# Kernel tuning notes

Hardware: AMD Instinct MI355X
Metric: run time of the kernel (lower is better)

## Reference

```python
import jax, jax.numpy as jnp
import numpy as np
from jax import lax


def setup_inputs() -> dict:
    key = jax.random.key(0)
    ks = jax.random.split(key, 5)
    B, N, F = 16, 2048, 64
    S, P, O = 4, 22, 42  # n_dimensions, n_propagate, n_filters
    x = jax.random.normal(ks[0], (B, N, F), dtype=jnp.float32)
    W_s = jax.random.normal(ks[1], (F, S), dtype=jnp.float32) * (1.0 / np.sqrt(F))
    b_s = jnp.zeros((S,), dtype=jnp.float32)
    W_f = jax.random.normal(ks[2], (F, P), dtype=jnp.float32) * (1.0 / np.sqrt(F))
    b_f = jnp.zeros((P,), dtype=jnp.float32)
    W_o = jax.random.normal(ks[3], (F + 2 * P, O), dtype=jnp.float32) * (1.0 / np.sqrt(F + 2 * P))
    b_o = jnp.zeros((O,), dtype=jnp.float32)
    return {"x": x, "W_s": W_s, "b_s": b_s, "W_f": W_f, "b_f": b_f,
            "W_o": W_o, "b_o": b_o, "n_neighbours": 40}


def reference(x, W_s, b_s, W_f, b_f, W_o, b_o, n_neighbours):
    # x: [B, N, F]
    coords = x @ W_s + b_s            # [B, N, S]   spatial transform
    feats = x @ W_f + b_f             # [B, N, P]   feature transform (FLR)
    # pairwise squared distances: [B, N, N]
    d2 = jnp.sum((coords[:, :, None, :] - coords[:, None, :, :]) ** 2, axis=-1)
    # k nearest (top_k of -distance); drop self (slot 0)
    neg_d, idx = lax.top_k(-d2, n_neighbours)        # [B, N, k]
    dist = -neg_d[:, :, 1:]                          # [B, N, k-1]
    nbr_idx = idx[:, :, 1:]                          # [B, N, k-1]
    weights = jnp.exp(-dist)[..., None]              # [B, N, k-1, 1]
    # batched gather of neighbour features: [B, N, k-1, P]
    nbr_feats = jax.vmap(lambda f, i: f[i])(feats, nbr_idx)
    weighted = nbr_feats * weights
    n_max = jnp.max(weighted, axis=2)                # [B, N, P]
    n_mean = jnp.mean(weighted, axis=2)              # [B, N, P]
    updated = jnp.concatenate([x, n_max, n_mean], axis=-1)  # [B, N, F+2P]
    return jnp.tanh(updated @ W_o + b_o)             # [B, N, n_filters]
```

## Files before the change

kernel.cpp:

```cpp
#include <hip/hip_runtime.h>
#include <math.h>

#define BB 16
#define NN 2048
#define FF 64
#define SS 4
#define PP 22
#define OO 42
#define FPDIM (FF + 2*PP)
#define NREG 32
#define PREBLK 128
#define XWOBLK ((BB*NN*21 + 255)/256)

__device__ __forceinline__ float readfirstlane_f32(float v) {
    return __uint_as_float((unsigned)__builtin_amdgcn_readfirstlane((int)__float_as_uint(v)));
}

__device__ __forceinline__ int wave_scan_dpp(int x) {
    x += __builtin_amdgcn_update_dpp(0, x, 0x111, 0xf, 0xf, true);
    x += __builtin_amdgcn_update_dpp(0, x, 0x112, 0xf, 0xf, true);
    x += __builtin_amdgcn_update_dpp(0, x, 0x114, 0xf, 0xf, true);
    x += __builtin_amdgcn_update_dpp(0, x, 0x118, 0xf, 0xf, true);
    x += __builtin_amdgcn_update_dpp(0, x, 0x142, 0xa, 0xf, true);
    x += __builtin_amdgcn_update_dpp(0, x, 0x143, 0xc, 0xf, true);
    return x;
}
__device__ __forceinline__ int wave_sum_dpp(int x) {
    return __builtin_amdgcn_readlane(wave_scan_dpp(x), 63);
}
__device__ __forceinline__ float wave_fsum_dpp(float x) {
    float t;
    t = __uint_as_float((unsigned)__builtin_amdgcn_update_dpp(0, (int)__float_as_uint(x), 0x111, 0xf, 0xf, true)); x += t;
    t = __uint_as_float((unsigned)__builtin_amdgcn_update_dpp(0, (int)__float_as_uint(x), 0x112, 0xf, 0xf, true)); x += t;
    t = __uint_as_float((unsigned)__builtin_amdgcn_update_dpp(0, (int)__float_as_uint(x), 0x114, 0xf, 0xf, true)); x += t;
    t = __uint_as_float((unsigned)__builtin_amdgcn_update_dpp(0, (int)__float_as_uint(x), 0x118, 0xf, 0xf, true)); x += t;
    t = __uint_as_float((unsigned)__builtin_amdgcn_update_dpp(0, (int)__float_as_uint(x), 0x142, 0xa, 0xf, true)); x += t;
    t = __uint_as_float((unsigned)__builtin_amdgcn_update_dpp(0, (int)__float_as_uint(x), 0x143, 0xc, 0xf, true)); x += t;
    return __uint_as_float((unsigned)__builtin_amdgcn_readlane((int)__float_as_uint(x), 63));
}

__global__ __launch_bounds__(256) void prep_kernel(
    const float* __restrict__ x, const float* __restrict__ Ws, const float* __restrict__ bs,
    const float* __restrict__ Wf, const float* __restrict__ bf,
    const float* __restrict__ Wo, const float* __restrict__ bo,
    float* __restrict__ coords, float* __restrict__ feats, float* __restrict__ xwo)
{
    if (blockIdx.x >= PREBLK) {
        int idx = (blockIdx.x - PREBLK) * 256 + threadIdx.x;
        if (idx >= BB * NN * 21) return;
        int row = idx / 21;
        int p   = idx - row * 21;
        int o   = p * 2;
        const float4* xr = (const float4*)(x + (size_t)row * FF);
        float a0 = bo[o], b0 = bo[o + 1], a1 = 0.f, b1 = 0.f;
        #pragma unroll
        for (int k4 = 0; k4 < FF / 4; k4++) {
            float4 xv = xr[k4];
            const float* wb = Wo + (k4 * 4) * OO + o;
            float2 w0 = *((const float2*)(wb));
            float2 w1 = *((const float2*)(wb + OO));
            float2 w2 = *((const float2*)(wb + 2 * OO));
            float2 w3 = *((const float2*)(wb + 3 * OO));
            a0 = fmaf(xv.x, w0.x, a0); b0 = fmaf(xv.x, w0.y, b0);
            a1 = fmaf(xv.y, w1.x, a1); b1 = fmaf(xv.y, w1.y, b1);
            a0 = fmaf(xv.z, w2.x, a0); b0 = fmaf(xv.z, w2.y, b0);
            a1 = fmaf(xv.w, w3.x, a1); b1 = fmaf(xv.w, w3.y, b1);
        }
        *((float2*)(xwo + (size_t)idx * 2)) = make_float2(a0 + a1, b0 + b1);
        return;
    }

    int row = blockIdx.x * 256 + threadIdx.x;
    if (row >= BB * NN) return;

    const float4* x4 = (const float4*)(x + (size_t)row * FF);
    float c0 = bs[0], c1 = bs[1], c2 = bs[2], c3 = bs[3];
    float f[PP];
    #pragma unroll
    for (int c = 0; c < PP; c++) f[c] = bf[c];

    #pragma unroll
    for (int k4 = 0; k4 < FF / 4; k4++) {
        float4 xv = x4[k4];
        float xs[4] = {xv.x, xv.y, xv.z, xv.w};
        #pragma unroll
        for (int r = 0; r < 4; r++) {
            int k = k4 * 4 + r;
            float xk = xs[r];
            c0 = fmaf(xk, Ws[k * SS + 0], c0);
            c1 = fmaf(xk, Ws[k * SS + 1], c1);
            c2 = fmaf(xk, Ws[k * SS + 2], c2);
            c3 = fmaf(xk, Ws[k * SS + 3], c3);
            #pragma unroll
            for (int c = 0; c < PP; c++) f[c] = fmaf(xk, Wf[k * PP + c], f[c]);
        }
    }
    float4* cp = (float4*)(coords + (size_t)row * SS);
    *cp = make_float4(c0, c1, c2, c3);
    float* fo = feats + (size_t)row * PP;
    #pragma unroll
    for (int c = 0; c < PP; c++) fo[c] = f[c];
}

__global__ __launch_bounds__(128, 4) void knn_out_kernel(
    const float* __restrict__ coords, const float* __restrict__ feats,
    const float* __restrict__ xwo, const float* __restrict__ Wo,
    const int* __restrict__ nnbr, float* __restrict__ out)
{
    const int lane = threadIdx.x & 63;
    const int w    = threadIdx.x >> 6;
    const int q    = blockIdx.x * 2 + w;
    const int b    = q >> 11;
    const int i    = q & (NN - 1);

    int K = *nnbr; K = K < 2 ? 2 : (K > 64 ? 64 : K);

    __shared__ int   isel[2][64];
    __shared__ float wsel[2][64];
    __shared__ unsigned long long candk[2][64];
    __shared__ __align__(16) float urow[2][48];

    float xw = 0.f;
    if (lane < OO) xw = xwo[(size_t)q * OO + lane];

    const float4* cb = (const float4*)(coords + (size_t)b * NN * SS);
    float4 qv = cb[i];
    const float qx = readfirstlane_f32(qv.x);
    const float qy = readfirstlane_f32(qv.y);
    const float qz = readfirstlane_f32(qv.z);
    const float qw = readfirstlane_f32(qv.w);

    float d2r[NREG];
    float lmin = INFINITY;
    #pragma unroll 4
    for (int r = 0; r < NREG; r++) {
        float4 c = cb[r * 64 + lane];
        float d0 = qx - c.x, d1 = qy - c.y, d2 = qz - c.z, d3 = qw - c.w;
        float v = d0 * d0 + d1 * d1 + d2 * d2 + d3 * d3;
        d2r[r] = v;
        lmin = fminf(lmin, v);
    }

    float t0 = wave_fsum_dpp(lmin) * (1.0f / 64.0f);

    unsigned loU = 0u, hiU = 0x7F800000u;
    int cLo = 0, cHi = NN;
    int laneLo = 0, laneHi = NREG;
    float tPrev = t0; int cPrev = -1;

    if (t0 > 1e-30f) {
        float t1 = t0 * 0.75f, t2 = t0 * 0.95f, t3 = t0 * 1.15f, t4 = t0 * 1.40f;
        int l1 = 0, l2 = 0, l3 = 0, l4 = 0;
        #pragma unroll
        for (int r = 0; r < NREG; r++) {
            float v = d2r[r];
            l1 += (v < t1) ? 1 : 0;
            l2 += (v < t2) ? 1 : 0;
            l3 += (v < t3) ? 1 : 0;
            l4 += (v < t4) ? 1 : 0;
        }
        int s12 = wave_sum_dpp(l1 | (l2 << 16));
        int s34 = wave_sum_dpp(l3 | (l4 << 16));
        int c1 = s12 & 0xFFFF, c2 = s12 >> 16, c3 = s34 & 0xFFFF, c4 = s34 >> 16;
        if (c1 >= K)      { hiU = __float_as_uint(t1); cHi = c1; laneHi = l1; }
        else if (c2 >= K) { loU = __float_as_uint(t1); cLo = c1; laneLo = l1;
                            hiU = __float_as_uint(t2); cHi = c2; laneHi = l2; }
        else if (c3 >= K) { loU = __float_as_uint(t2); cLo = c2; laneLo = l2;
                            hiU = __float_as_uint(t3); cHi = c3; laneHi = l3; }
        else if (c4 >= K) { loU = __float_as_uint(t3); cLo = c3; laneLo = l3;
                            hiU = __float_as_uint(t4); cHi = c4; laneHi = l4; }
        else              { loU = __float_as_uint(t4); cLo = c4; laneLo = l4; }
        int bc = -1, bd = 0x7FFFFFFF; float bt = t0;
        int cs[4] = {c1, c2, c3, c4}; float ts[4] = {t1, t2, t3, t4};
        #pragma unroll
        for (int u = 0; u < 4; u++) {
            int d = cs[u] > K ? cs[u] - K : K - cs[u];
            if (cs[u] > 0 && d < bd) { bd = d; bc = cs[u]; bt = ts[u]; }
        }
        if (bc > 0) { tPrev = bt; cPrev = bc; }
        else        { tPrev = t4; cPrev = 0; }
    }

    int probes = 0;
    while (cHi - cLo > 64 && hiU - loU > 1u && probes < 20) {
        unsigned tAU = 0u, tBU = 0u;
        bool fell = false;
        if (cPrev > 0) {
            float g = tPrev * __fsqrt_rn((float)K / (float)cPrev);
            tAU = __float_as_uint(g * 0.88f); tBU = __float_as_uint(g * 1.18f);
        } else if (cPrev == 0) {
            tAU = __float_as_uint(tPrev * 3.0f); tBU = __float_as_uint(tPrev * 9.0f);
        } else fell = true;
        unsigned span = hiU - loU;
        if (fell || !(tAU > loU && tAU < hiU)) tAU = loU + span / 3u;
        if (tAU <= loU) tAU = loU + 1u;
        if (tAU >= hiU) tAU = hiU - 1u;
        if (fell || !(tBU >= tAU && tBU < hiU)) tBU = tAU + (hiU - tAU) / 2u;
        if (tBU < tAU) tBU = tAU;
        if (tBU >= hiU) tBU = hiU - 1u;

        float tA = __uint_as_float(tAU), tB = __uint_as_float(tBU);
        int clA = 0, clB = 0;
        #pragma unroll
        for (int r = 0; r < NREG; r++) {
            clA += (d2r[r] < tA) ? 1 : 0;
            clB += (d2r[r] < tB) ? 1 : 0;
        }
        int tot = wave_sum_dpp(clA | (clB << 16));
        int cA = tot & 0xFFFF, cB = tot >> 16;

        if (cA >= K) { hiU = tAU; cHi = cA; laneHi = clA; }
        else {
            loU = tAU; cLo = cA; laneLo = clA;
            if (cB >= K) { hiU = tBU; cHi = cB; laneHi = clB; }
            else         { loU = tBU; cLo = cB; laneLo = clB; }
        }
        int dA = cA > K ? cA - K : K - cA;
        int dB = cB > K ? cB - K : K - cB;
        if (cA > 0 && dA <= dB) { tPrev = tA; cPrev = cA; }
        else                    { tPrev = tB; cPrev = cB; }
        probes++;
    }

    const float lo = __uint_as_float(loU);
    const float hi = __uint_as_float(hiU);
    const int  need = K - cLo;

    int c1c = laneLo;
    int c2c = laneHi - laneLo;
    if (lane == (i & 63) && loU > 0u) c1c -= 1;
    int pk = c1c | (c2c << 16);
    int inc = wave_scan_dpp(pk);
    int excl = inc - pk;
    int tot  = __builtin_amdgcn_readlane(inc, 63);
    int b1 = excl & 0xFFFF;
    int b2 = excl >> 16;
    const int nbelow = tot & 0xFFFF;
    int ecand = tot >> 16; if (ecand > 64) ecand = 64;
    #pragma unroll
    for (int r = 0; r < NREG; r++) {
        float v = d2r[r];
        int j = r * 64 + lane;
        if ((v < lo) & (j != i)) { isel[w][b1] = j; wsel[w][b1] = v; b1++; }
        else if ((v >= lo) & (v < hi)) { if (b2 < 64) candk[w][b2] = ((unsigned long long)__float_as_uint(v) << 32) | (unsigned)j; b2++; }
    }
    __builtin_amdgcn_wave_barrier();

    int nsel;
    if (ecand == need && loU > 0u) {
        if (lane < ecand) {
            int slot = nbelow + lane;
            if (slot < 64) {
                unsigned long long k2 = candk[w][lane];
                isel[w][slot] = (int)(k2 & 0xFFFFFFFFull);
                wsel[w][slot] = __uint_as_float((unsigned)(k2 >> 32));
            }
        }
        nsel = nbelow + ecand;
        if (nsel > 64) nsel = 64;
    } else {
        unsigned long long mykey = ~0ull;
        if (lane < ecand) mykey = candk[w][lane];
        int mr = 0;
        for (int u = 0; u < ecand; u++) {
            unsigned long long k2 = candk[w][u];
            mr += (k2 < mykey) ? 1 : 0;
        }
        int mj = (int)(mykey & 0xFFFFFFFFull);
        bool ps = (lane < ecand) & (mr < need) & (mj != i);
        unsigned long long ms = __ballot(ps);
        if (ps) {
            int slot = nbelow + __popcll(ms & ((1ull << lane) - 1ull));
            if (slot < 64) { isel[w][slot] = mj; wsel[w][slot] = __uint_as_float((unsigned)(mykey >> 32)); }
        }
        nsel = nbelow + __popcll(ms);
        if (nsel > 64) nsel = 64;
    }
    __builtin_amdgcn_wave_barrier();
    if (lane < nsel) wsel[w][lane] = __expf(-wsel[w][lane]);
    __builtin_amdgcn_wave_barrier();

    const float* fb = feats + (size_t)b * NN * PP;
    int g = lane >> 5, c = lane & 31;
    float mx = -INFINITY, sm = 0.f;
    if (c < PP) {
        #pragma unroll 8
        for (int m = g; m < nsel; m += 2) {
            int j = isel[w][m]; float wt = wsel[w][m];
            float f = fb[(size_t)j * PP + c];
            float wf = wt * f;
            mx = fmaxf(mx, wf); sm += wf;
        }
    }
    float mx2 = __shfl_xor(mx, 32, 64);
    float sm2 = __shfl_xor(sm, 32, 64);
    mx = fmaxf(mx, mx2); sm += sm2;
    if (g == 0 && c < PP) {
        urow[w][c]      = mx;
        urow[w][PP + c] = sm / (float)(K - 1);
    }
    __builtin_amdgcn_wave_barrier();

    if (lane < OO) {
        float a0 = xw, a1 = 0.f, a2 = 0.f, a3 = 0.f;
        const float* wo = Wo + FF * OO + lane;
        #pragma unroll
        for (int k4 = 0; k4 < (2 * PP) / 4; k4++) {
            float4 u = *((const float4*)&urow[w][k4 * 4]);
            a0 = fmaf(u.x, wo[(k4 * 4 + 0) * OO], a0);
            a1 = fmaf(u.y, wo[(k4 * 4 + 1) * OO], a1);
            a2 = fmaf(u.z, wo[(k4 * 4 + 2) * OO], a2);
            a3 = fmaf(u.w, wo[(k4 * 4 + 3) * OO], a3);
        }
        float acc = (a0 + a1) + (a2 + a3);
        float a = acc < -12.f ? -12.f : (acc > 12.f ? 12.f : acc);
        float e2 = __expf(2.f * a);
        out[(size_t)q * OO + lane] = (e2 - 1.f) / (e2 + 1.f);
    }
}

extern "C" void kernel_launch(void* const* d_in, const int* in_sizes, int n_in,
                              void* d_out, int out_size, void* d_ws, size_t ws_size,
                              hipStream_t stream) {
    const float* x  = (const float*)d_in[0];
    const float* Ws = (const float*)d_in[1];
    const float* bs = (const float*)d_in[2];
    const float* Wf = (const float*)d_in[3];
    const float* bf = (const float*)d_in[4];
    const float* Wo = (const float*)d_in[5];
    const float* bo = (const float*)d_in[6];
    const int*   nn = (const int*)d_in[7];
    float* out = (float*)d_out;

    float* coords = (float*)d_ws;
    float* feats  = coords + (size_t)BB * NN * SS;
    float* xwo    = feats  + (size_t)BB * NN * PP;

    prep_kernel<<<PREBLK + XWOBLK, 256, 0, stream>>>(x, Ws, bs, Wf, bf, Wo, bo, coords, feats, xwo);
    knn_out_kernel<<<(BB * NN) / 2, 128, 0, stream>>>(coords, feats, xwo, Wo, nn, out);
}
```

Baseline: 183.2 us.

## Replace threshold probing with ballot-compacted candidate list and in-register bisection

Reworks the per-query k-nearest selection. A single pass over the register distances compacts every candidate under a coarse threshold into a shared list of up to 256 packed (distance, index) keys using ballot and mbcnt. The threshold is refined by interpolation and bisection over only those few candidates held in registers, instead of repeated full 2048-element count passes with DPP reductions. Selected neighbours are stored as packed keys with precomputed feature offsets, which merges the index and weight arrays. The risk is extra capture iterations over all distances when the initial threshold guess yields fewer than K or more than 256 candidates.

```diff
diff --git a/kernel.cpp b/kernel.cpp
--- a/kernel.cpp
+++ b/kernel.cpp
@@ -9,6 +9,7 @@
 #define OO 42
 #define FPDIM (FF + 2*PP)
 #define NREG 32
+#define CAP 256
 #define PREBLK 128
 #define XWOBLK ((BB*NN*21 + 255)/256)
 
@@ -16,18 +17,11 @@
     return __uint_as_float((unsigned)__builtin_amdgcn_readfirstlane((int)__float_as_uint(v)));
 }
 
-__device__ __forceinline__ int wave_scan_dpp(int x) {
-    x += __builtin_amdgcn_update_dpp(0, x, 0x111, 0xf, 0xf, true);
-    x += __builtin_amdgcn_update_dpp(0, x, 0x112, 0xf, 0xf, true);
-    x += __builtin_amdgcn_update_dpp(0, x, 0x114, 0xf, 0xf, true);
-    x += __builtin_amdgcn_update_dpp(0, x, 0x118, 0xf, 0xf, true);
-    x += __builtin_amdgcn_update_dpp(0, x, 0x142, 0xa, 0xf, true);
-    x += __builtin_amdgcn_update_dpp(0, x, 0x143, 0xc, 0xf, true);
-    return x;
-}
-__device__ __forceinline__ int wave_sum_dpp(int x) {
-    return __builtin_amdgcn_readlane(wave_scan_dpp(x), 63);
-}
+__device__ __forceinline__ int lane_prefix(unsigned long long m) {
+    return __builtin_amdgcn_mbcnt_hi((unsigned)(m >> 32),
+           __builtin_amdgcn_mbcnt_lo((unsigned)m, 0u));
+}
+
 __device__ __forceinline__ float wave_fsum_dpp(float x) {
     float t;
     t = __uint_as_float((unsigned)__builtin_amdgcn_update_dpp(0, (int)__float_as_uint(x), 0x111, 0xf, 0xf, true)); x += t;
@@ -115,9 +109,9 @@
 
     int K = *nnbr; K = K < 2 ? 2 : (K > 64 ? 64 : K);
 
-    __shared__ int   isel[2][64];
-    __shared__ float wsel[2][64];
+    __shared__ unsigned long long list[2][CAP];
     __shared__ unsigned long long candk[2][64];
+    __shared__ unsigned long long selk[2][64];
     __shared__ __align__(16) float urow[2][48];
 
     float xw = 0.f;
@@ -142,152 +136,140 @@
     }
 
     float t0 = wave_fsum_dpp(lmin) * (1.0f / 64.0f);
-
-    unsigned loU = 0u, hiU = 0x7F800000u;
-    int cLo = 0, cHi = NN;
-    int laneLo = 0, laneHi = NREG;
-    float tPrev = t0; int cPrev = -1;
-
-    if (t0 > 1e-30f) {
-        float t1 = t0 * 0.75f, t2 = t0 * 0.95f, t3 = t0 * 1.15f, t4 = t0 * 1.40f;
-        int l1 = 0, l2 = 0, l3 = 0, l4 = 0;
+    if (!(t0 > 1e-30f)) t0 = 1e-30f;
+
+    unsigned tinU = __float_as_uint(t0);
+    unsigned tcU  = __float_as_uint(t0 * 1.5f);
+    unsigned bLoU = 0u;
+    unsigned bHiU = 0x7F800000u;
+    int c_in = 0, c_tc = 0;
+
+    for (int att = 0; att < 40; att++) {
+        int sb = 0, ci = 0;
         #pragma unroll
         for (int r = 0; r < NREG; r++) {
-            float v = d2r[r];
-            l1 += (v < t1) ? 1 : 0;
-            l2 += (v < t2) ? 1 : 0;
-            l3 += (v < t3) ? 1 : 0;
-            l4 += (v < t4) ? 1 : 0;
-        }
-        int s12 = wave_sum_dpp(l1 | (l2 << 16));
-        int s34 = wave_sum_dpp(l3 | (l4 << 16));
-        int c1 = s12 & 0xFFFF, c2 = s12 >> 16, c3 = s34 & 0xFFFF, c4 = s34 >> 16;
-        if (c1 >= K)      { hiU = __float_as_uint(t1); cHi = c1; laneHi = l1; }
-        else if (c2 >= K) { loU = __float_as_uint(t1); cLo = c1; laneLo = l1;
-                            hiU = __float_as_uint(t2); cHi = c2; laneHi = l2; }
-        else if (c3 >= K) { loU = __float_as_uint(t2); cLo = c2; laneLo = l2;
-                            hiU = __float_as_uint(t3); cHi = c3; laneHi = l3; }
-        else if (c4 >= K) { loU = __float_as_uint(t3); cLo = c3; laneLo = l3;
-                            hiU = __float_as_uint(t4); cHi = c4; laneHi = l4; }
-        else              { loU = __float_as_uint(t4); cLo = c4; laneLo = l4; }
-        int bc = -1, bd = 0x7FFFFFFF; float bt = t0;
-        int cs[4] = {c1, c2, c3, c4}; float ts[4] = {t1, t2, t3, t4};
-        #pragma unroll
-        for (int u = 0; u < 4; u++) {
-            int d = cs[u] > K ? cs[u] - K : K - cs[u];
-            if (cs[u] > 0 && d < bd) { bd = d; bc = cs[u]; bt = ts[u]; }
-        }
-        if (bc > 0) { tPrev = bt; cPrev = bc; }
-        else        { tPrev = t4; cPrev = 0; }
-    }
-
-    int probes = 0;
-    while (cHi - cLo > 64 && hiU - loU > 1u && probes < 20) {
-        unsigned tAU = 0u, tBU = 0u;
-        bool fell = false;
-        if (cPrev > 0) {
-            float g = tPrev * __fsqrt_rn((float)K / (float)cPrev);
-            tAU = __float_as_uint(g * 0.88f); tBU = __float_as_uint(g * 1.18f);
-        } else if (cPrev == 0) {
-            tAU = __float_as_uint(tPrev * 3.0f); tBU = __float_as_uint(tPrev * 9.0f);
-        } else fell = true;
-        unsigned span = hiU - loU;
-        if (fell || !(tAU > loU && tAU < hiU)) tAU = loU + span / 3u;
-        if (tAU <= loU) tAU = loU + 1u;
-        if (tAU >= hiU) tAU = hiU - 1u;
-        if (fell || !(tBU >= tAU && tBU < hiU)) tBU = tAU + (hiU - tAU) / 2u;
-        if (tBU < tAU) tBU = tAU;
-        if (tBU >= hiU) tBU = hiU - 1u;
-
-        float tA = __uint_as_float(tAU), tB = __uint_as_float(tBU);
-        int clA = 0, clB = 0;
-        #pragma unroll
-        for (int r = 0; r < NREG; r++) {
-            clA += (d2r[r] < tA) ? 1 : 0;
-            clB += (d2r[r] < tB) ? 1 : 0;
-        }
-        int tot = wave_sum_dpp(clA | (clB << 16));
-        int cA = tot & 0xFFFF, cB = tot >> 16;
-
-        if (cA >= K) { hiU = tAU; cHi = cA; laneHi = clA; }
-        else {
-            loU = tAU; cLo = cA; laneLo = clA;
-            if (cB >= K) { hiU = tBU; cHi = cB; laneHi = clB; }
-            else         { loU = tBU; cLo = cB; laneLo = clB; }
-        }
-        int dA = cA > K ? cA - K : K - cA;
-        int dB = cB > K ? cB - K : K - cB;
-        if (cA > 0 && dA <= dB) { tPrev = tA; cPrev = cA; }
-        else                    { tPrev = tB; cPrev = cB; }
-        probes++;
-    }
-
-    const float lo = __uint_as_float(loU);
-    const float hi = __uint_as_float(hiU);
-    const int  need = K - cLo;
-
-    int c1c = laneLo;
-    int c2c = laneHi - laneLo;
-    if (lane == (i & 63) && loU > 0u) c1c -= 1;
-    int pk = c1c | (c2c << 16);
-    int inc = wave_scan_dpp(pk);
-    int excl = inc - pk;
-    int tot  = __builtin_amdgcn_readlane(inc, 63);
-    int b1 = excl & 0xFFFF;
-    int b2 = excl >> 16;
-    const int nbelow = tot & 0xFFFF;
-    int ecand = tot >> 16; if (ecand > 64) ecand = 64;
+            unsigned vb = __float_as_uint(d2r[r]);
+            ci += (int)__popcll(__ballot(vb < tinU));
+            unsigned long long m = __ballot(vb < tcU);
+            if (vb < tcU) {
+                int pos = sb + lane_prefix(m);
+                if (pos < CAP)
+                    list[w][pos] = ((unsigned long long)vb << 32) | (unsigned)(r * 64 + lane);
+            }
+            sb += (int)__popcll(m);
+        }
+        c_in = ci; c_tc = sb;
+        if (c_tc >= K && c_tc <= CAP) break;
+        if (c_tc < K) {
+            bLoU = tcU; tinU = tcU;
+            unsigned prop = __float_as_uint(__uint_as_float(tcU) * 3.0f);
+            if (prop <= bLoU || prop >= bHiU) prop = bLoU + ((bHiU - bLoU) >> 1);
+            if (prop <= bLoU) prop = bLoU + 1u;
+            tcU = prop;
+        } else {
+            bHiU = tcU;
+            unsigned prop = __float_as_uint(__uint_as_float(tcU) * 0.55f);
+            if (prop <= bLoU || prop >= bHiU) prop = bLoU + ((bHiU - bLoU) >> 1);
+            if (prop <= bLoU) prop = bLoU + 1u;
+            tcU = prop;
+            unsigned pin = __float_as_uint(__uint_as_float(tcU) * 0.62f);
+            tinU = (pin < tcU) ? pin : (tcU - 1u);
+        }
+    }
+    __builtin_amdgcn_wave_barrier();
+
+    unsigned loU, hiU; int cLo, cHi;
+    if (c_in >= K) { loU = 0u;   cLo = 0;    hiU = tinU; cHi = c_in; }
+    else           { loU = tinU; cLo = c_in; hiU = tcU;  cHi = c_tc; }
+
+    unsigned long long k0 = ~0ull, k1 = ~0ull, k2 = ~0ull, k3 = ~0ull;
+    if (lane < c_tc)       k0 = list[w][lane];
+    if (lane + 64 < c_tc)  k1 = list[w][lane + 64];
+    if (c_tc > 128) {
+        if (lane + 128 < c_tc) k2 = list[w][lane + 128];
+        if (lane + 192 < c_tc) k3 = list[w][lane + 192];
+    }
+
+    int guard = 0;
+    while (cHi - cLo > 64 && hiU - loU > 1u && guard < 24) {
+        unsigned tmU;
+        if (guard & 1) {
+            tmU = loU + ((hiU - loU) >> 1);
+        } else {
+            float tLo = __uint_as_float(loU), tHi = __uint_as_float(hiU);
+            float frac = (float)(K - cLo) / (float)(cHi - cLo);
+            tmU = __float_as_uint(tLo + (tHi - tLo) * frac);
+        }
+        if (tmU <= loU) tmU = loU + 1u;
+        if (tmU >= hiU) tmU = hiU - 1u;
+        int cm = (int)__popcll(__ballot((unsigned)(k0 >> 32) < tmU))
+               + (int)__popcll(__ballot((unsigned)(k1 >> 32) < tmU))
+               + (int)__popcll(__ballot((unsigned)(k2 >> 32) < tmU))
+               + (int)__popcll(__ballot((unsigned)(k3 >> 32) < tmU));
+        if (cm >= K) { hiU = tmU; cHi = cm; } else { loU = tmU; cLo = cm; }
+        guard++;
+    }
+
+    int nbelow = 0, ecand = 0;
     #pragma unroll
-    for (int r = 0; r < NREG; r++) {
-        float v = d2r[r];
-        int j = r * 64 + lane;
-        if ((v < lo) & (j != i)) { isel[w][b1] = j; wsel[w][b1] = v; b1++; }
-        else if ((v >= lo) & (v < hi)) { if (b2 < 64) candk[w][b2] = ((unsigned long long)__float_as_uint(v) << 32) | (unsigned)j; b2++; }
-    }
-    __builtin_amdgcn_wave_barrier();
-
-    int nsel;
-    if (ecand == need && loU > 0u) {
-        if (lane < ecand) {
-            int slot = nbelow + lane;
-            if (slot < 64) {
-                unsigned long long k2 = candk[w][lane];
-                isel[w][slot] = (int)(k2 & 0xFFFFFFFFull);
-                wsel[w][slot] = __uint_as_float((unsigned)(k2 >> 32));
-            }
-        }
-        nsel = nbelow + ecand;
-        if (nsel > 64) nsel = 64;
-    } else {
-        unsigned long long mykey = ~0ull;
-        if (lane < ecand) mykey = candk[w][lane];
-        int mr = 0;
-        for (int u = 0; u < ecand; u++) {
-            unsigned long long k2 = candk[w][u];
-            mr += (k2 < mykey) ? 1 : 0;
-        }
-        int mj = (int)(mykey & 0xFFFFFFFFull);
-        bool ps = (lane < ecand) & (mr < need) & (mj != i);
-        unsigned long long ms = __ballot(ps);
-        if (ps) {
-            int slot = nbelow + __popcll(ms & ((1ull << lane) - 1ull));
-            if (slot < 64) { isel[w][slot] = mj; wsel[w][slot] = __uint_as_float((unsigned)(mykey >> 32)); }
-        }
-        nsel = nbelow + __popcll(ms);
-        if (nsel > 64) nsel = 64;
-    }
-    __builtin_amdgcn_wave_barrier();
-    if (lane < nsel) wsel[w][lane] = __expf(-wsel[w][lane]);
-    __builtin_amdgcn_wave_barrier();
-
-    const float* fb = feats + (size_t)b * NN * PP;
-    int g = lane >> 5, c = lane & 31;
+    for (int t = 0; t < 4; t++) {
+        unsigned long long kk = (t == 0) ? k0 : (t == 1) ? k1 : (t == 2) ? k2 : k3;
+        unsigned hb = (unsigned)(kk >> 32);
+        unsigned jj = (unsigned)kk;
+        bool isb = (hb < loU) & (jj != (unsigned)i);
+        bool isc = (hb >= loU) & (hb < hiU);
+        unsigned long long mb = __ballot(isb);
+        unsigned long long mc = __ballot(isc);
+        if (isb) {
+            int s = nbelow + lane_prefix(mb);
+            if (s < 64) selk[w][s] = ((unsigned long long)hb << 32) | (unsigned)(jj * PP);
+        }
+        if (isc) {
+            int s = ecand + lane_prefix(mc);
+            if (s < 64) candk[w][s] = kk;
+        }
+        nbelow += (int)__popcll(mb);
+        ecand  += (int)__popcll(mc);
+    }
+    if (ecand > 64) ecand = 64;
+    __builtin_amdgcn_wave_barrier();
+
+    const int need = K - cLo;
+    unsigned long long mykey = ~0ull;
+    if (lane < ecand) mykey = candk[w][lane];
+    int mr = 0;
+    for (int u = 0; u < ecand; u++) {
+        unsigned long long ku = candk[w][u];
+        mr += (ku < mykey) ? 1 : 0;
+    }
+    unsigned mj = (unsigned)mykey;
+    bool ps = (lane < ecand) & (mr < need) & (mj != (unsigned)i);
+    unsigned long long ms = __ballot(ps);
+    if (ps) {
+        int slot = nbelow + lane_prefix(ms);
+        if (slot < 64)
+            selk[w][slot] = (mykey & 0xFFFFFFFF00000000ull) | (unsigned)(mj * PP);
+    }
+    int nsel = nbelow + (int)__popcll(ms);
+    if (nsel > 64) nsel = 64;
+    __builtin_amdgcn_wave_barrier();
+
+    if (lane < nsel) {
+        unsigned* su = (unsigned*)&selk[w][0];
+        float d = __uint_as_float(su[2 * lane + 1]);
+        su[2 * lane + 1] = __float_as_uint(__expf(-d));
+    }
+    __builtin_amdgcn_wave_barrier();
+
+    const int g = lane >> 5, c = lane & 31;
+    const float* fbc = feats + (size_t)b * NN * PP + c;
     float mx = -INFINITY, sm = 0.f;
     if (c < PP) {
-        #pragma unroll 8
+        #pragma unroll 4
         for (int m = g; m < nsel; m += 2) {
-            int j = isel[w][m]; float wt = wsel[w][m];
-            float f = fb[(size_t)j * PP + c];
+            unsigned long long e = selk[w][m];
+            float wt = __uint_as_float((unsigned)(e >> 32));
+            float f  = fbc[(unsigned)e];
             float wf = wt * f;
             mx = fmaxf(mx, wf); sm += wf;
         }
```

New measurement: 230.2 us. 1.26x slower.

## Fuse x·Wo projection into prep rows and use ballot counting in kNN

Applied to the files above, without the earlier changes.

The prep kernel now computes the x·Wo partial projection per row, reusing the same x reads. Wo is staged in LDS, so the separate 2688-block xwo launch section goes away. In the kNN kernel, the per-lane counts plus DPP packed scans are replaced by ballot/popcount threshold counts and mbcnt-based compaction. This cuts redundant x loads and scan latency, but each prep thread now holds 44 more accumulators, which raises register pressure. Prep parallelism is also limited to only 128 blocks.

```diff
diff --git a/kernel.cpp b/kernel.cpp
--- a/kernel.cpp
+++ b/kernel.cpp
@@ -10,24 +10,16 @@
 #define FPDIM (FF + 2*PP)
 #define NREG 32
 #define PREBLK 128
-#define XWOBLK ((BB*NN*21 + 255)/256)
 
 __device__ __forceinline__ float readfirstlane_f32(float v) {
     return __uint_as_float((unsigned)__builtin_amdgcn_readfirstlane((int)__float_as_uint(v)));
 }
 
-__device__ __forceinline__ int wave_scan_dpp(int x) {
-    x += __builtin_amdgcn_update_dpp(0, x, 0x111, 0xf, 0xf, true);
-    x += __builtin_amdgcn_update_dpp(0, x, 0x112, 0xf, 0xf, true);
-    x += __builtin_amdgcn_update_dpp(0, x, 0x114, 0xf, 0xf, true);
-    x += __builtin_amdgcn_update_dpp(0, x, 0x118, 0xf, 0xf, true);
-    x += __builtin_amdgcn_update_dpp(0, x, 0x142, 0xa, 0xf, true);
-    x += __builtin_amdgcn_update_dpp(0, x, 0x143, 0xc, 0xf, true);
-    return x;
-}
-__device__ __forceinline__ int wave_sum_dpp(int x) {
-    return __builtin_amdgcn_readlane(wave_scan_dpp(x), 63);
-}
+__device__ __forceinline__ int lane_prefix(unsigned long long m) {
+    return __builtin_amdgcn_mbcnt_hi((unsigned)(m >> 32),
+           __builtin_amdgcn_mbcnt_lo((unsigned)m, 0u));
+}
+
 __device__ __forceinline__ float wave_fsum_dpp(float x) {
     float t;
     t = __uint_as_float((unsigned)__builtin_amdgcn_update_dpp(0, (int)__float_as_uint(x), 0x111, 0xf, 0xf, true)); x += t;
@@ -45,39 +37,30 @@
     const float* __restrict__ Wo, const float* __restrict__ bo,
     float* __restrict__ coords, float* __restrict__ feats, float* __restrict__ xwo)
 {
-    if (blockIdx.x >= PREBLK) {
-        int idx = (blockIdx.x - PREBLK) * 256 + threadIdx.x;
-        if (idx >= BB * NN * 21) return;
-        int row = idx / 21;
-        int p   = idx - row * 21;
-        int o   = p * 2;
-        const float4* xr = (const float4*)(x + (size_t)row * FF);
-        float a0 = bo[o], b0 = bo[o + 1], a1 = 0.f, b1 = 0.f;
-        #pragma unroll
-        for (int k4 = 0; k4 < FF / 4; k4++) {
-            float4 xv = xr[k4];
-            const float* wb = Wo + (k4 * 4) * OO + o;
-            float2 w0 = *((const float2*)(wb));
-            float2 w1 = *((const float2*)(wb + OO));
-            float2 w2 = *((const float2*)(wb + 2 * OO));
-            float2 w3 = *((const float2*)(wb + 3 * OO));
-            a0 = fmaf(xv.x, w0.x, a0); b0 = fmaf(xv.x, w0.y, b0);
-            a1 = fmaf(xv.y, w1.x, a1); b1 = fmaf(xv.y, w1.y, b1);
-            a0 = fmaf(xv.z, w2.x, a0); b0 = fmaf(xv.z, w2.y, b0);
-            a1 = fmaf(xv.w, w3.x, a1); b1 = fmaf(xv.w, w3.y, b1);
-        }
-        *((float2*)(xwo + (size_t)idx * 2)) = make_float2(a0 + a1, b0 + b1);
-        return;
-    }
-
-    int row = blockIdx.x * 256 + threadIdx.x;
-    if (row >= BB * NN) return;
+    __shared__ float woLds[64 * 44];
+
+    {
+        int wrow = threadIdx.x >> 2, quarter = threadIdx.x & 3;
+        #pragma unroll
+        for (int u = 0; u < 11; u++) {
+            int c = quarter * 11 + u;
+            float v = (c < OO) ? Wo[wrow * OO + c] : 0.f;
+            woLds[wrow * 44 + c] = v;
+        }
+    }
+    __syncthreads();
+
+    const int row = blockIdx.x * 256 + threadIdx.x;
 
     const float4* x4 = (const float4*)(x + (size_t)row * FF);
     float c0 = bs[0], c1 = bs[1], c2 = bs[2], c3 = bs[3];
     float f[PP];
     #pragma unroll
     for (int c = 0; c < PP; c++) f[c] = bf[c];
+    float4 wa[11];
+    #pragma unroll
+    for (int c4 = 0; c4 < 10; c4++) wa[c4] = *((const float4*)(bo + c4 * 4));
+    wa[10] = make_float4(bo[40], bo[41], 0.f, 0.f);
 
     #pragma unroll
     for (int k4 = 0; k4 < FF / 4; k4++) {
@@ -93,6 +76,15 @@
             c3 = fmaf(xk, Ws[k * SS + 3], c3);
             #pragma unroll
             for (int c = 0; c < PP; c++) f[c] = fmaf(xk, Wf[k * PP + c], f[c]);
+            const float4* wrow = (const float4*)(woLds + k * 44);
+            #pragma unroll
+            for (int c4 = 0; c4 < 11; c4++) {
+                float4 wv = wrow[c4];
+                wa[c4].x = fmaf(xk, wv.x, wa[c4].x);
+                wa[c4].y = fmaf(xk, wv.y, wa[c4].y);
+                wa[c4].z = fmaf(xk, wv.z, wa[c4].z);
+                wa[c4].w = fmaf(xk, wv.w, wa[c4].w);
+            }
         }
     }
     float4* cp = (float4*)(coords + (size_t)row * SS);
@@ -100,6 +92,13 @@
     float* fo = feats + (size_t)row * PP;
     #pragma unroll
     for (int c = 0; c < PP; c++) fo[c] = f[c];
+    float* xo = xwo + (size_t)row * OO;
+    #pragma unroll
+    for (int c4 = 0; c4 < 10; c4++) {
+        *((float2*)(xo + c4 * 4))     = make_float2(wa[c4].x, wa[c4].y);
+        *((float2*)(xo + c4 * 4 + 2)) = make_float2(wa[c4].z, wa[c4].w);
+    }
+    *((float2*)(xo + 40)) = make_float2(wa[10].x, wa[10].y);
 }
 
 __global__ __launch_bounds__(128, 4) void knn_out_kernel(
@@ -145,31 +144,27 @@
 
     unsigned loU = 0u, hiU = 0x7F800000u;
     int cLo = 0, cHi = NN;
-    int laneLo = 0, laneHi = NREG;
     float tPrev = t0; int cPrev = -1;
 
     if (t0 > 1e-30f) {
         float t1 = t0 * 0.75f, t2 = t0 * 0.95f, t3 = t0 * 1.15f, t4 = t0 * 1.40f;
-        int l1 = 0, l2 = 0, l3 = 0, l4 = 0;
+        int c1 = 0, c2 = 0, c3 = 0, c4 = 0;
         #pragma unroll
         for (int r = 0; r < NREG; r++) {
             float v = d2r[r];
-            l1 += (v < t1) ? 1 : 0;
-            l2 += (v < t2) ? 1 : 0;
-            l3 += (v < t3) ? 1 : 0;
-            l4 += (v < t4) ? 1 : 0;
-        }
-        int s12 = wave_sum_dpp(l1 | (l2 << 16));
-        int s34 = wave_sum_dpp(l3 | (l4 << 16));
-        int c1 = s12 & 0xFFFF, c2 = s12 >> 16, c3 = s34 & 0xFFFF, c4 = s34 >> 16;
-        if (c1 >= K)      { hiU = __float_as_uint(t1); cHi = c1; laneHi = l1; }
-        else if (c2 >= K) { loU = __float_as_uint(t1); cLo = c1; laneLo = l1;
-                            hiU = __float_as_uint(t2); cHi = c2; laneHi = l2; }
-        else if (c3 >= K) { loU = __float_as_uint(t2); cLo = c2; laneLo = l2;
-                            hiU = __float_as_uint(t3); cHi = c3; laneHi = l3; }
-        else if (c4 >= K) { loU = __float_as_uint(t3); cLo = c3; laneLo = l3;
-                            hiU = __float_as_uint(t4); cHi = c4; laneHi = l4; }
-        else              { loU = __float_as_uint(t4); cLo = c4; laneLo = l4; }
+            c1 += (int)__popcll(__ballot(v < t1));
+            c2 += (int)__popcll(__ballot(v < t2));
+            c3 += (int)__popcll(__ballot(v < t3));
+            c4 += (int)__popcll(__ballot(v < t4));
+        }
+        if (c1 >= K)      { hiU = __float_as_uint(t1); cHi = c1; }
+        else if (c2 >= K) { loU = __float_as_uint(t1); cLo = c1;
+                            hiU = __float_as_uint(t2); cHi = c2; }
+        else if (c3 >= K) { loU = __float_as_uint(t2); cLo = c2;
+                            hiU = __float_as_uint(t3); cHi = c3; }
+        else if (c4 >= K) { loU = __float_as_uint(t3); cLo = c3;
+                            hiU = __float_as_uint(t4); cHi = c4; }
+        else              { loU = __float_as_uint(t4); cLo = c4; }
         int bc = -1, bd = 0x7FFFFFFF; float bt = t0;
         int cs[4] = {c1, c2, c3, c4}; float ts[4] = {t1, t2, t3, t4};
         #pragma unroll
@@ -200,20 +195,19 @@
         if (tBU >= hiU) tBU = hiU - 1u;
 
         float tA = __uint_as_float(tAU), tB = __uint_as_float(tBU);
-        int clA = 0, clB = 0;
+        int cA = 0, cB = 0;
         #pragma unroll
         for (int r = 0; r < NREG; r++) {
-            clA += (d2r[r] < tA) ? 1 : 0;
-            clB += (d2r[r] < tB) ? 1 : 0;
-        }
-        int tot = wave_sum_dpp(clA | (clB << 16));
-        int cA = tot & 0xFFFF, cB = tot >> 16;
-
-        if (cA >= K) { hiU = tAU; cHi = cA; laneHi = clA; }
+            float v = d2r[r];
+            cA += (int)__popcll(__ballot(v < tA));
+            cB += (int)__popcll(__ballot(v < tB));
+        }
+
+        if (cA >= K) { hiU = tAU; cHi = cA; }
         else {
-            loU = tAU; cLo = cA; laneLo = clA;
-            if (cB >= K) { hiU = tBU; cHi = cB; laneHi = clB; }
-            else         { loU = tBU; cLo = cB; laneLo = clB; }
+            loU = tAU; cLo = cA;
+            if (cB >= K) { hiU = tBU; cHi = cB; }
+            else         { loU = tBU; cLo = cB; }
         }
         int dA = cA > K ? cA - K : K - cA;
         int dB = cB > K ? cB - K : K - cB;
@@ -226,24 +220,27 @@
     const float hi = __uint_as_float(hiU);
     const int  need = K - cLo;
 
-    int c1c = laneLo;
-    int c2c = laneHi - laneLo;
-    if (lane == (i & 63) && loU > 0u) c1c -= 1;
-    int pk = c1c | (c2c << 16);
-    int inc = wave_scan_dpp(pk);
-    int excl = inc - pk;
-    int tot  = __builtin_amdgcn_readlane(inc, 63);
-    int b1 = excl & 0xFFFF;
-    int b2 = excl >> 16;
-    const int nbelow = tot & 0xFFFF;
-    int ecand = tot >> 16; if (ecand > 64) ecand = 64;
+    int nbelow = 0, ecand = 0;
     #pragma unroll
     for (int r = 0; r < NREG; r++) {
         float v = d2r[r];
         int j = r * 64 + lane;
-        if ((v < lo) & (j != i)) { isel[w][b1] = j; wsel[w][b1] = v; b1++; }
-        else if ((v >= lo) & (v < hi)) { if (b2 < 64) candk[w][b2] = ((unsigned long long)__float_as_uint(v) << 32) | (unsigned)j; b2++; }
-    }
+        bool isB = (v < lo) & (j != i);
+        bool isC = (v >= lo) & (v < hi);
+        unsigned long long mB = __ballot(isB);
+        unsigned long long mC = __ballot(isC);
+        if (isB) {
+            int s = nbelow + lane_prefix(mB);
+            isel[w][s] = j; wsel[w][s] = v;
+        }
+        if (isC) {
+            int s = ecand + lane_prefix(mC);
+            if (s < 64) candk[w][s] = ((unsigned long long)__float_as_uint(v) << 32) | (unsigned)j;
+        }
+        nbelow += (int)__popcll(mB);
+        ecand  += (int)__popcll(mC);
+    }
+    if (ecand > 64) ecand = 64;
     __builtin_amdgcn_wave_barrier();
 
     int nsel;
@@ -336,6 +333,6 @@
     float* feats  = coords + (size_t)BB * NN * SS;
     float* xwo    = feats  + (size_t)BB * NN * PP;
 
-    prep_kernel<<<PREBLK + XWOBLK, 256, 0, stream>>>(x, Ws, bs, Wf, bf, Wo, bo, coords, feats, xwo);
+    prep_kernel<<<PREBLK, 256, 0, stream>>>(x, Ws, bs, Wf, bf, Wo, bo, coords, feats, xwo);
     knn_out_kernel<<<(BB * NN) / 2, 128, 0, stream>>>(coords, feats, xwo, Wo, nn, out);
 }
```

New measurement: 190.9 us. +4.2%, slower.

## Restructure x@Wo precompute to stage transposed Wo in LDS and row-per-lane

Applied to the files above, without the earlier changes.

The x·Wo partial projection in the prep kernel now gives each block 64 rows. Each block stages a transposed, padded copy of Wo in shared memory, and each lane keeps its whole x row in registers while its wave computes a slice of the output columns. Results go through an LDS buffer so the global store is coalesced as float4. This removes the redundant per-thread reloads of the x row and the scattered global weight loads, at the cost of more LDS, more registers and two block barriers.

```diff
diff --git a/kernel.cpp b/kernel.cpp
--- a/kernel.cpp
+++ b/kernel.cpp
@@ -10,7 +10,8 @@
 #define FPDIM (FF + 2*PP)
 #define NREG 32
 #define PREBLK 128
-#define XWOBLK ((BB*NN*21 + 255)/256)
+#define XWOBLK 512
+#define WOPAD 68
 
 __device__ __forceinline__ float readfirstlane_f32(float v) {
     return __uint_as_float((unsigned)__builtin_amdgcn_readfirstlane((int)__float_as_uint(v)));
@@ -45,28 +46,52 @@
     const float* __restrict__ Wo, const float* __restrict__ bo,
     float* __restrict__ coords, float* __restrict__ feats, float* __restrict__ xwo)
 {
+    __shared__ float woT[OO * WOPAD];
+    __shared__ float obuf[64 * OO];
+
     if (blockIdx.x >= PREBLK) {
-        int idx = (blockIdx.x - PREBLK) * 256 + threadIdx.x;
-        if (idx >= BB * NN * 21) return;
-        int row = idx / 21;
-        int p   = idx - row * 21;
-        int o   = p * 2;
+        const int xblk = blockIdx.x - PREBLK;
+        const int r0   = xblk * 64;
+        const int lane = threadIdx.x & 63;
+        const int wv   = threadIdx.x >> 6;
+
+        for (int idx = threadIdx.x; idx < 64 * OO; idx += 256) {
+            int k = idx / OO;
+            int o = idx - k * OO;
+            woT[o * WOPAD + k] = Wo[idx];
+        }
+        __syncthreads();
+
+        const int row = r0 + lane;
         const float4* xr = (const float4*)(x + (size_t)row * FF);
-        float a0 = bo[o], b0 = bo[o + 1], a1 = 0.f, b1 = 0.f;
-        #pragma unroll
-        for (int k4 = 0; k4 < FF / 4; k4++) {
-            float4 xv = xr[k4];
-            const float* wb = Wo + (k4 * 4) * OO + o;
-            float2 w0 = *((const float2*)(wb));
-            float2 w1 = *((const float2*)(wb + OO));
-            float2 w2 = *((const float2*)(wb + 2 * OO));
-            float2 w3 = *((const float2*)(wb + 3 * OO));
-            a0 = fmaf(xv.x, w0.x, a0); b0 = fmaf(xv.x, w0.y, b0);
-            a1 = fmaf(xv.y, w1.x, a1); b1 = fmaf(xv.y, w1.y, b1);
-            a0 = fmaf(xv.z, w2.x, a0); b0 = fmaf(xv.z, w2.y, b0);
-            a1 = fmaf(xv.w, w3.x, a1); b1 = fmaf(xv.w, w3.y, b1);
-        }
-        *((float2*)(xwo + (size_t)idx * 2)) = make_float2(a0 + a1, b0 + b1);
+        float4 xv[16];
+        #pragma unroll
+        for (int k4 = 0; k4 < 16; k4++) xv[k4] = xr[k4];
+
+        const int cbase = wv * 11;
+        const int nc = (wv == 3) ? 9 : 11;
+        #pragma unroll
+        for (int u = 0; u < 11; u++) {
+            if (u < nc) {
+                int o = cbase + u;
+                float a0 = bo[o], a1 = 0.f, a2 = 0.f, a3 = 0.f;
+                const float4* wt = (const float4*)(woT + o * WOPAD);
+                #pragma unroll
+                for (int k4 = 0; k4 < 16; k4++) {
+                    float4 wv4 = wt[k4];
+                    a0 = fmaf(xv[k4].x, wv4.x, a0);
+                    a1 = fmaf(xv[k4].y, wv4.y, a1);
+                    a2 = fmaf(xv[k4].z, wv4.z, a2);
+                    a3 = fmaf(xv[k4].w, wv4.w, a3);
+                }
+                obuf[lane * OO + o] = (a0 + a1) + (a2 + a3);
+            }
+        }
+        __syncthreads();
+
+        const float4* ob4 = (const float4*)obuf;
+        float4* gout = (float4*)(xwo + (size_t)r0 * OO);
+        for (int t = threadIdx.x; t < (64 * OO) / 4; t += 256) gout[t] = ob4[t];
         return;
     }
 
```

After: 173.3 us. -5.4%, faster.
